# Performance work log

Hardware: AMD Instinct MI355X
Metric: run time of the kernel (lower is better)

Reference implementation:

```python
import jax, jax.numpy as jnp
import numpy as np

N = 100000   # nodes
E = 1600000  # edges
D = 128      # input_dim == hidden_dim
G = 64       # graphs in batch
EPS = 1e-5


def setup_inputs() -> dict:
    key = jax.random.key(0)
    ks = jax.random.split(key, 16)
    s = 1.0 / np.sqrt(D)
    inp = {
        "x": jax.random.normal(ks[0], (N, D), jnp.float32),
        "edge_index": jax.random.randint(ks[1], (2, E), 0, N, jnp.int64),
        "batch": jnp.sort(jax.random.randint(ks[2], (N,), 0, G, jnp.int64)),
        # 4 blocks x 2 SAGEConv layers = 8 convs, all DxD
        "Wl": jax.random.normal(ks[3], (8, D, D), jnp.float32) * s,
        "bl": jnp.zeros((8, D), jnp.float32),
        "Wr": jax.random.normal(ks[4], (8, D, D), jnp.float32) * s,
        "gamma": jnp.ones((4, D), jnp.float32),
        "beta": jnp.zeros((4, D), jnp.float32),
        # classifier: 2D -> D -> D//2 -> 1
        "W1": jax.random.normal(ks[5], (2 * D, D), jnp.float32) / np.sqrt(2 * D),
        "b1": jnp.zeros((D,), jnp.float32),
        "W2": jax.random.normal(ks[6], (D, D // 2), jnp.float32) * s,
        "b2": jnp.zeros((D // 2,), jnp.float32),
        "W3": jax.random.normal(ks[7], (D // 2, 1), jnp.float32) / np.sqrt(D // 2),
        "b3": jnp.zeros((1,), jnp.float32),
    }
    return inp


def _sage_conv(h, src, dst, inv_deg, W_l, b_l, W_r):
    # mean-aggregate neighbor features (messages flow src -> dst)
    agg = jax.ops.segment_sum(h[src], dst, num_segments=N) * inv_deg
    return agg @ W_l + b_l + h @ W_r


def _forward(x, edge_index, batch, Wl, bl, Wr, gamma, beta, W1, b1, W2, b2, W3, b3):
    src, dst = edge_index[0], edge_index[1]
    deg = jax.ops.segment_sum(jnp.ones((E,), x.dtype), dst, num_segments=N)
    inv_deg = (1.0 / jnp.maximum(deg, 1.0))[:, None]  # [N,1]

    h = x
    for blk in range(4):
        # GraphSAGE(in, hid, num_layers=2): conv -> relu -> conv
        h = _sage_conv(h, src, dst, inv_deg, Wl[2 * blk], bl[2 * blk], Wr[2 * blk])
        h = jax.nn.relu(h)
        h = _sage_conv(h, src, dst, inv_deg, Wl[2 * blk + 1], bl[2 * blk + 1], Wr[2 * blk + 1])
        # BatchNorm1d over nodes (training-mode batch statistics, biased var)
        mu = jnp.mean(h, axis=0)
        var = jnp.var(h, axis=0)
        h = (h - mu) * jax.lax.rsqrt(var + EPS) * gamma[blk] + beta[blk]
        h = jax.nn.relu(h)  # dropout is identity in eval mode

    # global mean / max pool over graph ids
    cnt = jax.ops.segment_sum(jnp.ones((N,), h.dtype), batch, num_segments=G)
    x_mean = jax.ops.segment_sum(h, batch, num_segments=G) / jnp.maximum(cnt, 1.0)[:, None]
    x_max = jax.ops.segment_max(h, batch, num_segments=G)
    g = jnp.concatenate([x_mean, x_max], axis=1)  # [G, 2D]

    g = jax.nn.relu(g @ W1 + b1)
    g = jax.nn.relu(g @ W2 + b2)
    return g @ W3 + b3  # [G, 1]


def reference(x, edge_index, batch, Wl, bl, Wr, gamma, beta, W1, b1, W2, b2, W3, b3):
    return _forward(x, edge_index, batch, Wl, bl, Wr, gamma, beta, W1, b1, W2, b2, W3, b3)
```

## Files before the change

kernel.cpp:

```cpp
#include <hip/hip_runtime.h>
#include <hip/hip_bf16.h>
#include <math.h>

#define NN 100000
#define NE 1600000
#define DIM 128
#define NG 64
#define EPSBN 1e-5f
#define NBLK 782
#define SORT_WIN 12500
#define NBINBLK 6250
#define DSL 64

typedef unsigned int u32;
typedef unsigned short u16;
typedef __attribute__((ext_vector_type(8))) short bf8_t;
typedef __attribute__((ext_vector_type(4))) float f4_t;
typedef __attribute__((ext_vector_type(4))) unsigned short u16x4;
#define MFMA(a, b, c) __builtin_amdgcn_mfma_f32_16x16x32_bf16((a), (b), (c), 0, 0, 0)

__device__ __forceinline__ u16 f2bf(float f) {
    u32 u = __float_as_uint(f);
    u32 r = u + 0x7FFFu + ((u >> 16) & 1u);
    return (u16)(r >> 16);
}
__device__ __forceinline__ float bf2f(u16 h) { return __uint_as_float(((u32)h) << 16); }

__global__ void k_bin_cnt(const int* __restrict__ ei, int* __restrict__ blkcnt) {
    __shared__ int c[8];
    int t = threadIdx.x;
    if (t < 8) c[t] = 0;
    __syncthreads();
    int e = blockIdx.x * 256 + t;
    int d = ei[NE + e];
    atomicAdd(&c[d / SORT_WIN], 1);
    __syncthreads();
    if (t < 8) blkcnt[blockIdx.x * 8 + t] = c[t];
}

__global__ void k_bin_scan(const int* __restrict__ blkcnt, int* __restrict__ blkoff,
                           int* __restrict__ wtotal) {
    __shared__ int ps[256];
    int w = blockIdx.x, t = threadIdx.x;
    const int PER = (NBINBLK + 255) / 256;
    int s = 0;
    for (int i = 0; i < PER; ++i) {
        int b = t * PER + i;
        if (b < NBINBLK) s += blkcnt[b * 8 + w];
    }
    ps[t] = s;
    for (int off = 1; off < 256; off <<= 1) {
        __syncthreads();
        int x = (t >= off) ? ps[t - off] : 0;
        __syncthreads();
        ps[t] += x;
    }
    __syncthreads();
    int run = (t ? ps[t - 1] : 0);
    for (int i = 0; i < PER; ++i) {
        int b = t * PER + i;
        if (b < NBINBLK) { blkoff[b * 8 + w] = run; run += blkcnt[b * 8 + w]; }
    }
    if (t == 255) wtotal[w] = ps[255];
}

__global__ void k_bin_start(const int* __restrict__ wtotal, int* __restrict__ binStart) {
    if (threadIdx.x == 0) {
        int a = 0;
        for (int w = 0; w < 8; ++w) { binStart[w] = a; a += wtotal[w]; }
        binStart[8] = a;
    }
}

__global__ void k_bin_place(const int* __restrict__ ei, const int* __restrict__ blkoff,
                            const int* __restrict__ binStart, int2* __restrict__ binned) {
    __shared__ int base[8];
    int t = threadIdx.x;
    if (t < 8) base[t] = binStart[t] + blkoff[blockIdx.x * 8 + t];
    __syncthreads();
    int e = blockIdx.x * 256 + t;
    int s = ei[e], d = ei[NE + e];
    int pos = atomicAdd(&base[d / SORT_WIN], 1);
    binned[pos] = make_int2(s, d);
}

__global__ void k_deg2(const int2* __restrict__ binned, const int* __restrict__ binStart,
                       int* __restrict__ deg) {
    int w = blockIdx.x & 7, sl = blockIdx.x >> 3;
    int b0 = binStart[w], b1 = binStart[w + 1];
    int chunk = (b1 - b0 + DSL - 1) / DSL;
    int r0 = b0 + sl * chunk, r1 = min(r0 + chunk, b1);
    for (int i = r0 + threadIdx.x; i < r1; i += 256)
        atomicAdd(&deg[binned[i].y], 1);
}

__global__ void k_scatter(const int2* __restrict__ binned, const int* __restrict__ binStart,
                          int* __restrict__ cursor, int* __restrict__ sorted_src) {
    int w = blockIdx.x & 7, sl = blockIdx.x >> 3;
    int b0 = binStart[w], b1 = binStart[w + 1];
    int chunk = (b1 - b0 + DSL - 1) / DSL;
    int r0 = b0 + sl * chunk, r1 = min(r0 + chunk, b1);
    for (int i = r0 + threadIdx.x; i < r1; i += 256) {
        int2 e = binned[i];
        int pos = atomicAdd(&cursor[e.y], 1);
        sorted_src[pos] = e.x;
    }
}

#define SCAN_B 256
__global__ void k_scan1(const int* __restrict__ deg, int* __restrict__ row_start,
                        int* __restrict__ bsum, float* __restrict__ inv_deg) {
    __shared__ int s[SCAN_B];
    int t = threadIdx.x;
    int i = blockIdx.x * SCAN_B + t;
    int v = (i < NN) ? deg[i] : 0;
    if (i < NN) inv_deg[i] = 1.0f / (float)(v > 1 ? v : 1);
    s[t] = v;
    for (int off = 1; off < SCAN_B; off <<= 1) {
        __syncthreads();
        int x = (t >= off) ? s[t - off] : 0;
        __syncthreads();
        s[t] += x;
    }
    if (i < NN) row_start[i + 1] = s[t];
    if (t == SCAN_B - 1) bsum[blockIdx.x] = s[t];
}

__global__ void k_scan2(int* __restrict__ bsum, int nb) {
    __shared__ int s[512];
    int t = threadIdx.x;
    int v = (t < nb) ? bsum[t] : 0;
    s[t] = v;
    for (int off = 1; off < 512; off <<= 1) {
        __syncthreads();
        int x = (t >= off) ? s[t - off] : 0;
        __syncthreads();
        s[t] += x;
    }
    if (t < nb) bsum[t] = s[t] - v;
}

__global__ void k_scan3(int* __restrict__ row_start, const int* __restrict__ bsum,
                        int* __restrict__ cursor) {
    int i = blockIdx.x * blockDim.x + threadIdx.x;
    if (i < NN) {
        int v = row_start[i + 1] + bsum[i / SCAN_B];
        row_start[i + 1] = v;
        if (i + 1 < NN) cursor[i + 1] = v;
    }
    if (i == 0) { row_start[0] = 0; cursor[0] = 0; }
}

__global__ void k_bounds(const int* __restrict__ batch, int* __restrict__ gs) {
    int g = threadIdx.x;
    if (g > NG) return;
    int lo = 0, hi = NN;
    while (lo < hi) {
        int mid = (lo + hi) >> 1;
        if (batch[mid] < g) lo = mid + 1; else hi = mid;
    }
    gs[g] = lo;
}

__global__ void k_split_x(const float* __restrict__ x, u16* __restrict__ Xh,
                          u16* __restrict__ Xl) {
    int idx = blockIdx.x * 256 + threadIdx.x;
    int base = idx * 4;
    float4 v = *reinterpret_cast<const float4*>(&x[base]);
    u16x4 hi, lo;
    float vv[4] = {v.x, v.y, v.z, v.w};
#pragma unroll
    for (int j = 0; j < 4; j++) {
        u16 h = f2bf(vv[j]);
        hi[j] = h;
        lo[j] = f2bf(vv[j] - bf2f(h));
    }
    *reinterpret_cast<u16x4*>(&Xh[base]) = hi;
    *reinterpret_cast<u16x4*>(&Xl[base]) = lo;
}

__global__ void k_prep_w(const float* __restrict__ Wl, const float* __restrict__ Wr,
                         u16* __restrict__ Wth, u16* __restrict__ Wtl) {
    int idx = blockIdx.x * 256 + threadIdx.x;
    int k = idx & 255;
    int col = (idx >> 8) & 127;
    int c = idx >> 15;
    float v = (k < 128) ? Wl[(c * 128 + k) * 128 + col] : Wr[(c * 128 + (k - 128)) * 128 + col];
    u16 h = f2bf(v);
    Wth[idx] = h;
    Wtl[idx] = f2bf(v - bf2f(h));
}

template <int AFF>
__global__ void k_aggregate(const u16* __restrict__ Hh,
                            const int* __restrict__ row_start, const int* __restrict__ ssrc,
                            const float* __restrict__ inv_deg, const float* __restrict__ ss,
                            u16* __restrict__ Ah, u16* __restrict__ Al) {
    int wid = blockIdx.x * 4 + (threadIdx.x >> 6);
    int lane = threadIdx.x & 63;
    int half = lane >> 5;
    int cl = lane & 31;
    if (wid >= NN) return;
    float sc0 = 0.f, sc1 = 0.f, sc2 = 0.f, sc3 = 0.f;
    float sh0 = 0.f, sh1 = 0.f, sh2 = 0.f, sh3 = 0.f;
    if (AFF) {
        float4 s4 = *reinterpret_cast<const float4*>(ss + cl * 4);
        float4 h4 = *reinterpret_cast<const float4*>(ss + 128 + cl * 4);
        sc0 = s4.x; sc1 = s4.y; sc2 = s4.z; sc3 = s4.w;
        sh0 = h4.x; sh1 = h4.y; sh2 = h4.z; sh3 = h4.w;
    }
    int beg = row_start[wid], end = row_start[wid + 1];
    int n = end - beg;
    float a0 = 0.f, a1 = 0.f, a2 = 0.f, a3 = 0.f;
#define ACCUM(vv)                                                                   \
    {                                                                               \
        float t0 = __uint_as_float((vv).x << 16);                                   \
        float t1 = __uint_as_float((vv).x & 0xFFFF0000u);                           \
        float t2 = __uint_as_float((vv).y << 16);                                   \
        float t3 = __uint_as_float((vv).y & 0xFFFF0000u);                           \
        if (AFF) {                                                                  \
            t0 = fmaxf(t0 * sc0 + sh0, 0.f); t1 = fmaxf(t1 * sc1 + sh1, 0.f);       \
            t2 = fmaxf(t2 * sc2 + sh2, 0.f); t3 = fmaxf(t3 * sc3 + sh3, 0.f);       \
        }                                                                           \
        a0 += t0; a1 += t1; a2 += t2; a3 += t3;                                     \
    }
    for (int base = 0; base < n; base += 64) {
        int rem = n - base;
        int idx = beg + base + (lane < rem ? lane : 0);
        int sv = ssrc[idx];
        int m = rem < 64 ? rem : 64;
        int j = 0;
        for (; j + 4 <= m; j += 4) {
            int sA = __shfl(sv, j + half);
            int sB = __shfl(sv, j + 2 + half);
            uint2 vA = *reinterpret_cast<const uint2*>(
                reinterpret_cast<const u32*>(Hh + (size_t)sA * DIM) + cl * 2);
            uint2 vB = *reinterpret_cast<const uint2*>(
                reinterpret_cast<const u32*>(Hh + (size_t)sB * DIM) + cl * 2);
            ACCUM(vA); ACCUM(vB);
        }
        for (; j < m; j += 2) {
            if (j + half < m) {
                int s0 = __shfl(sv, j + half);
                uint2 v = *reinterpret_cast<const uint2*>(
                    reinterpret_cast<const u32*>(Hh + (size_t)s0 * DIM) + cl * 2);
                ACCUM(v);
            }
        }
    }
#undef ACCUM
    a0 += __shfl_down(a0, 32);
    a1 += __shfl_down(a1, 32);
    a2 += __shfl_down(a2, 32);
    a3 += __shfl_down(a3, 32);
    if (half == 0) {
        float sc = inv_deg[wid];
        a0 *= sc; a1 *= sc; a2 *= sc; a3 *= sc;
        u16 h0 = f2bf(a0), h1 = f2bf(a1), h2 = f2bf(a2), h3 = f2bf(a3);
        u16 l0 = f2bf(a0 - bf2f(h0)), l1 = f2bf(a1 - bf2f(h1));
        u16 l2 = f2bf(a2 - bf2f(h2)), l3 = f2bf(a3 - bf2f(h3));
        uint2 hv = make_uint2((u32)h0 | ((u32)h1 << 16), (u32)h2 | ((u32)h3 << 16));
        uint2 lv = make_uint2((u32)l0 | ((u32)l1 << 16), (u32)l2 | ((u32)l3 << 16));
        *reinterpret_cast<uint2*>(Ah + (size_t)wid * DIM + cl * 4) = hv;
        *reinterpret_cast<uint2*>(Al + (size_t)wid * DIM + cl * 4) = lv;
    }
}

__device__ __forceinline__ void affine_split(bf8_t& h, bf8_t& l,
                                             const float* __restrict__ ss, int k0) {
#pragma unroll
    for (int j = 0; j < 8; ++j) {
        float v = bf2f((u16)h[j]) + bf2f((u16)l[j]);
        v = fmaxf(v * ss[k0 + j] + ss[128 + k0 + j], 0.f);
        u16 hh = f2bf(v);
        h[j] = (short)hh;
        l[j] = (short)f2bf(v - bf2f(hh));
    }
}

template <bool RELU, bool STATS, bool AFF2>
__global__ __launch_bounds__(256) void k_gemm(
    const u16* __restrict__ A1h, const u16* __restrict__ A1l,
    const u16* __restrict__ A2h, const u16* __restrict__ A2l,
    const u16* __restrict__ Wth, const u16* __restrict__ Wtl,
    const float* __restrict__ bias, const float* __restrict__ ss,
    u16* __restrict__ Oh, u16* __restrict__ Ol,
    float* __restrict__ partials) {
    __shared__ float cs[128], cq[128];
    int t = threadIdx.x;
    if (STATS) {
        if (t < 128) { cs[t] = 0.f; cq[t] = 0.f; }
        __syncthreads();
    }
    int w = t >> 6, l = t & 63;
    int rl = l & 15, kg = l >> 4;
    int rbase = blockIdx.x * 128 + w * 32;
    int row0 = rbase + rl, row1 = rbase + 16 + rl;
    int row0c = min(row0, NN - 1), row1c = min(row1, NN - 1);

    f4_t acc[2][8];
#pragma unroll
    for (int i = 0; i < 2; i++)
#pragma unroll
        for (int j = 0; j < 8; j++) acc[i][j] = (f4_t){0.f, 0.f, 0.f, 0.f};

#pragma unroll
    for (int ks = 0; ks < 4; ++ks) {
        int k0 = ks * 32 + kg * 8;
        bf8_t a0h = *reinterpret_cast<const bf8_t*>(A1h + row0c * DIM + k0);
        bf8_t a0l = *reinterpret_cast<const bf8_t*>(A1l + row0c * DIM + k0);
        bf8_t a1h = *reinterpret_cast<const bf8_t*>(A1h + row1c * DIM + k0);
        bf8_t a1l = *reinterpret_cast<const bf8_t*>(A1l + row1c * DIM + k0);
#pragma unroll
        for (int cf = 0; cf < 8; ++cf) {
            int wo = (cf * 16 + rl) * 256 + k0;
            bf8_t bh = *reinterpret_cast<const bf8_t*>(Wth + wo);
            bf8_t bl_ = *reinterpret_cast<const bf8_t*>(Wtl + wo);
            acc[0][cf] = MFMA(a0h, bh, acc[0][cf]);
            acc[0][cf] = MFMA(a0h, bl_, acc[0][cf]);
            acc[0][cf] = MFMA(a0l, bh, acc[0][cf]);
            acc[1][cf] = MFMA(a1h, bh, acc[1][cf]);
            acc[1][cf] = MFMA(a1h, bl_, acc[1][cf]);
            acc[1][cf] = MFMA(a1l, bh, acc[1][cf]);
        }
    }
#pragma unroll
    for (int ks = 0; ks < 4; ++ks) {
        int k0 = ks * 32 + kg * 8;
        bf8_t a0h = *reinterpret_cast<const bf8_t*>(A2h + row0c * DIM + k0);
        bf8_t a0l = *reinterpret_cast<const bf8_t*>(A2l + row0c * DIM + k0);
        bf8_t a1h = *reinterpret_cast<const bf8_t*>(A2h + row1c * DIM + k0);
        bf8_t a1l = *reinterpret_cast<const bf8_t*>(A2l + row1c * DIM + k0);
        if (AFF2) {
            affine_split(a0h, a0l, ss, k0);
            affine_split(a1h, a1l, ss, k0);
        }
#pragma unroll
        for (int cf = 0; cf < 8; ++cf) {
            int wo = (cf * 16 + rl) * 256 + 128 + k0;
            bf8_t bh = *reinterpret_cast<const bf8_t*>(Wth + wo);
            bf8_t bl_ = *reinterpret_cast<const bf8_t*>(Wtl + wo);
            acc[0][cf] = MFMA(a0h, bh, acc[0][cf]);
            acc[0][cf] = MFMA(a0h, bl_, acc[0][cf]);
            acc[0][cf] = MFMA(a0l, bh, acc[0][cf]);
            acc[1][cf] = MFMA(a1h, bh, acc[1][cf]);
            acc[1][cf] = MFMA(a1h, bl_, acc[1][cf]);
            acc[1][cf] = MFMA(a1l, bh, acc[1][cf]);
        }
    }

#pragma unroll
    for (int rf = 0; rf < 2; ++rf) {
        int rb = rbase + rf * 16 + kg * 4;
#pragma unroll
        for (int cf = 0; cf < 8; ++cf) {
            int col = cf * 16 + rl;
            float bv = bias[col];
            float s = 0.f, q = 0.f;
#pragma unroll
            for (int i = 0; i < 4; ++i) {
                int row = rb + i;
                float v = acc[rf][cf][i] + bv;
                if (RELU) v = fmaxf(v, 0.f);
                if (row < NN) {
                    u16 hi = f2bf(v);
                    Oh[row * DIM + col] = hi;
                    Ol[row * DIM + col] = f2bf(v - bf2f(hi));
                    if (STATS) { s += v; q += v * v; }
                }
            }
            if (STATS) {
                s += __shfl_xor(s, 16); s += __shfl_xor(s, 32);
                q += __shfl_xor(q, 16); q += __shfl_xor(q, 32);
                if (l < 16) {
                    atomicAdd(&cs[col], s);
                    atomicAdd(&cq[col], q);
                }
            }
        }
    }
    if (STATS) {
        __syncthreads();
        partials[blockIdx.x * 256 + t] = (t < 128) ? cs[t] : cq[t - 128];
    }
}

__global__ void k_bn_r1(const float* __restrict__ partials, float* __restrict__ colpart) {
    int t = threadIdx.x;
    int b = blockIdx.x;
    int b0 = b * 25, b1 = min(b0 + 25, NBLK);
    float s = 0.f;
    for (int i = b0; i < b1; ++i) s += partials[i * 256 + t];
    colpart[b * 256 + t] = s;
}

__global__ void k_bn_r2(const float* __restrict__ colpart, const float* __restrict__ gamma,
                        const float* __restrict__ beta, float* __restrict__ scaleshift) {
    __shared__ float sm[256];
    int t = threadIdx.x;
    float s = 0.f;
#pragma unroll
    for (int b = 0; b < 32; ++b) s += colpart[b * 256 + t];
    sm[t] = s;
    __syncthreads();
    if (t < 128) {
        float mu = sm[t] * (1.0f / NN);
        float var = sm[t + 128] * (1.0f / NN) - mu * mu;
        float sc = rsqrtf(var + EPSBN) * gamma[t];
        scaleshift[t] = sc;
        scaleshift[t + 128] = beta[t] - mu * sc;
    }
}

__global__ void k_pool(const u16* __restrict__ Hh, const int* __restrict__ gs,
                       const float* __restrict__ ss,
                       float* __restrict__ pSum, float* __restrict__ pMax) {
    int g = blockIdx.x >> 3, slice = blockIdx.x & 7;
    int s0 = gs[g], s1 = gs[g + 1];
    int len = s1 - s0;
    int chunk = (len + 7) >> 3;
    int r0 = s0 + slice * chunk;
    int r1 = min(r0 + chunk, s1);
    int t = threadIdx.x;
    int c2 = (t & 63) * 2, half = t >> 6;
    float sc0 = ss[c2], sc1 = ss[c2 + 1];
    float sh0 = ss[128 + c2], sh1 = ss[128 + c2 + 1];
    float sa = 0.f, sb = 0.f, ma = 0.f, mb = 0.f;
    for (int r = r0 + half; r < r1; r += 4) {
        u32 h2 = *reinterpret_cast<const u32*>(Hh + r * DIM + c2);
        float v0 = fmaxf(__uint_as_float(h2 << 16) * sc0 + sh0, 0.f);
        float v1 = fmaxf(__uint_as_float(h2 & 0xFFFF0000u) * sc1 + sh1, 0.f);
        sa += v0; sb += v1;
        ma = fmaxf(ma, v0); mb = fmaxf(mb, v1);
    }
    __shared__ float ls[4][128], lm[4][128];
    ls[half][c2] = sa; ls[half][c2 + 1] = sb;
    lm[half][c2] = ma; lm[half][c2 + 1] = mb;
    __syncthreads();
    if (t < 128) {
        float s = ls[0][t] + ls[1][t] + ls[2][t] + ls[3][t];
        float m = fmaxf(fmaxf(lm[0][t], lm[1][t]), fmaxf(lm[2][t], lm[3][t]));
        atomicAdd(&pSum[g * DIM + t], s);
        atomicMax((int*)&pMax[g * DIM + t], __float_as_int(m));
    }
}

__global__ void k_mlp(const float* __restrict__ pSum, const float* __restrict__ pMax,
                      const int* __restrict__ gs,
                      const float* __restrict__ W1, const float* __restrict__ b1,
                      const float* __restrict__ W2, const float* __restrict__ b2,
                      const float* __restrict__ W3, const float* __restrict__ b3,
                      float* __restrict__ out) {
    __shared__ float g[256], y1[128], y2[64];
    int gi = blockIdx.x;
    int t = threadIdx.x;
    int cnt = gs[gi + 1] - gs[gi];
    float inv = 1.0f / fmaxf((float)cnt, 1.0f);
    g[t] = pSum[gi * DIM + t] * inv;
    g[128 + t] = pMax[gi * DIM + t];
    __syncthreads();
    float a = b1[t];
    for (int k = 0; k < 256; k++) a += g[k] * W1[k * 128 + t];
    y1[t] = fmaxf(a, 0.f);
    __syncthreads();
    if (t < 64) {
        float a2 = b2[t];
        for (int k = 0; k < 128; k++) a2 += y1[k] * W2[k * 64 + t];
        y2[t] = fmaxf(a2, 0.f);
    }
    __syncthreads();
    if (t < 64) {
        float p = y2[t] * W3[t];
#pragma unroll
        for (int off = 32; off; off >>= 1) p += __shfl_down(p, off);
        if (t == 0) out[gi] = p + b3[0];
    }
}

extern "C" void kernel_launch(void* const* d_in, const int* in_sizes, int n_in,
                              void* d_out, int out_size, void* d_ws, size_t ws_size,
                              hipStream_t stream) {
    const float* x     = (const float*)d_in[0];
    const int*   ei    = (const int*)d_in[1];
    const int*   batch = (const int*)d_in[2];
    const float* Wl    = (const float*)d_in[3];
    const float* bl    = (const float*)d_in[4];
    const float* Wr    = (const float*)d_in[5];
    const float* gamma = (const float*)d_in[6];
    const float* beta  = (const float*)d_in[7];
    const float* W1    = (const float*)d_in[8];
    const float* b1    = (const float*)d_in[9];
    const float* W2    = (const float*)d_in[10];
    const float* b2    = (const float*)d_in[11];
    const float* W3    = (const float*)d_in[12];
    const float* b3    = (const float*)d_in[13];
    float* out = (float*)d_out;

    char* p = (char*)d_ws;
    size_t off = 0;
    auto alloc = [&](size_t bytes) -> void* {
        void* r = p + off;
        off += (bytes + 255) & ~(size_t)255;
        return r;
    };
    const size_t HB = (size_t)NN * DIM * 2;
    u16* Xh   = (u16*)alloc(HB);
    u16* Xl   = (u16*)alloc(HB);
    u16* hAh  = (u16*)alloc(HB);
    u16* hAl  = (u16*)alloc(HB);
    u16* aggh = (u16*)alloc(HB);
    u16* aggl = (u16*)alloc(HB);
    int*   ssrc      = (int*)alloc((size_t)NE * 4);
    u16*   Wth       = (u16*)alloc((size_t)8 * 128 * 256 * 2);
    u16*   Wtl       = (u16*)alloc((size_t)8 * 128 * 256 * 2);
    float* partials  = (float*)alloc((size_t)NBLK * 256 * 4);
    float* colpart   = (float*)alloc(32 * 256 * 4);
    int*   deg       = (int*)alloc(NN * 4);
    float* inv_deg   = (float*)alloc(NN * 4);
    int*   row_start = (int*)alloc((NN + 1) * 4);
    int*   cursor    = (int*)alloc(NN * 4);
    int*   bsum      = (int*)alloc(512 * 4);
    int*   gs        = (int*)alloc((NG + 1) * 4);
    int*   blkcnt    = (int*)alloc((size_t)NBINBLK * 8 * 4);
    int*   blkoff    = (int*)alloc((size_t)NBINBLK * 8 * 4);
    int*   wtotal    = (int*)alloc(8 * 4);
    int*   binStart  = (int*)alloc(9 * 4);
    float* ssb       = (float*)alloc(4 * 256 * 4);
    float* pSum      = (float*)alloc(NG * DIM * 4);
    float* pMax      = (float*)alloc(NG * DIM * 4);
    int2*  binned    = (int2*)aggh;

    const int nbN = (NN + 255) / 256;
    const int nbQ = NN * DIM / 4 / 256;
    const int aggGrid = (NN + 3) / 4;

    hipMemsetAsync(deg, 0, NN * 4, stream);
    k_bin_cnt<<<NBINBLK, 256, 0, stream>>>(ei, blkcnt);
    k_bin_scan<<<8, 256, 0, stream>>>(blkcnt, blkoff, wtotal);
    k_bin_start<<<1, 64, 0, stream>>>(wtotal, binStart);
    k_bin_place<<<NBINBLK, 256, 0, stream>>>(ei, blkoff, binStart, binned);
    k_deg2<<<8 * DSL, 256, 0, stream>>>(binned, binStart, deg);
    k_scan1<<<nbN, 256, 0, stream>>>(deg, row_start, bsum, inv_deg);
    k_scan2<<<1, 512, 0, stream>>>(bsum, nbN);
    k_scan3<<<nbN, 256, 0, stream>>>(row_start, bsum, cursor);
    k_scatter<<<8 * DSL, 256, 0, stream>>>(binned, binStart, cursor, ssrc);
    k_bounds<<<1, 128, 0, stream>>>(batch, gs);

    k_split_x<<<nbQ, 256, 0, stream>>>(x, Xh, Xl);
    k_prep_w<<<8 * 128 * 256 / 256, 256, 0, stream>>>(Wl, Wr, Wth, Wtl);

    for (int b = 0; b < 4; b++) {
        int c0 = 2 * b, c1 = 2 * b + 1;
        const u16* W0h = Wth + (size_t)c0 * 128 * 256;
        const u16* W0l = Wtl + (size_t)c0 * 128 * 256;
        const u16* W1h = Wth + (size_t)c1 * 128 * 256;
        const u16* W1l = Wtl + (size_t)c1 * 128 * 256;
        const float* ssPrev = ssb + (size_t)(b > 0 ? b - 1 : 0) * 256;
        if (b == 0) {
            k_aggregate<0><<<aggGrid, 256, 0, stream>>>(Xh, row_start, ssrc, inv_deg,
                                                        ssPrev, aggh, aggl);
            k_gemm<true, false, false><<<NBLK, 256, 0, stream>>>(
                aggh, aggl, Xh, Xl, W0h, W0l, bl + c0 * DIM, ssPrev, hAh, hAl, partials);
        } else {
            k_aggregate<1><<<aggGrid, 256, 0, stream>>>(Xh, row_start, ssrc, inv_deg,
                                                        ssPrev, aggh, aggl);
            k_gemm<true, false, true><<<NBLK, 256, 0, stream>>>(
                aggh, aggl, Xh, Xl, W0h, W0l, bl + c0 * DIM, ssPrev, hAh, hAl, partials);
        }
        k_aggregate<0><<<aggGrid, 256, 0, stream>>>(hAh, row_start, ssrc, inv_deg,
                                                    ssPrev, aggh, aggl);
        k_gemm<false, true, false><<<NBLK, 256, 0, stream>>>(
            aggh, aggl, hAh, hAl, W1h, W1l, bl + c1 * DIM, ssPrev, Xh, Xl, partials);
        k_bn_r1<<<32, 256, 0, stream>>>(partials, colpart);
        k_bn_r2<<<1, 256, 0, stream>>>(colpart, gamma + b * DIM, beta + b * DIM,
                                       ssb + (size_t)b * 256);
    }

    hipMemsetAsync(pSum, 0, NG * DIM * 4, stream);
    hipMemsetAsync(pMax, 0, NG * DIM * 4, stream);
    k_pool<<<NG * 8, 256, 0, stream>>>(Xh, gs, ssb + 3 * 256, pSum, pMax);
    k_mlp<<<NG, 128, 0, stream>>>(pSum, pMax, gs, W1, b1, W2, b2, W3, b3, out);
}
```

Baseline: 1.662 ms.

## Restructure GEMM tiling: per-wave column slices with register-resident weights and double-buffered A loads

The GEMM kernel now gives each block 64 rows, and each of its four waves a 32-column slice, instead of each wave owning 32 rows and all 128 columns. Each wave keeps its weight slice (hi/lo bf16, full K=256) in registers, and the A-operand loads are double-buffered across K chunks so loads overlap with MFMA work. The grid doubles to 1563 blocks with a 2-blocks-per-CU launch bound, and the BN partial reduction is resized to match. This trades repeated weight reloads for higher register pressure and reading each A row from four waves.

```diff
diff --git a/kernel.cpp b/kernel.cpp
--- a/kernel.cpp
+++ b/kernel.cpp
@@ -7,7 +7,7 @@
 #define DIM 128
 #define NG 64
 #define EPSBN 1e-5f
-#define NBLK 782
+#define NGB 1563
 #define SORT_WIN 12500
 #define NBINBLK 6250
 #define DSL 64
@@ -279,7 +279,7 @@
 }
 
 template <bool RELU, bool STATS, bool AFF2>
-__global__ __launch_bounds__(256) void k_gemm(
+__global__ __launch_bounds__(256, 2) void k_gemm(
     const u16* __restrict__ A1h, const u16* __restrict__ A1l,
     const u16* __restrict__ A2h, const u16* __restrict__ A2l,
     const u16* __restrict__ Wth, const u16* __restrict__ Wtl,
@@ -288,107 +288,124 @@
     float* __restrict__ partials) {
     __shared__ float cs[128], cq[128];
     int t = threadIdx.x;
-    if (STATS) {
-        if (t < 128) { cs[t] = 0.f; cq[t] = 0.f; }
-        __syncthreads();
-    }
     int w = t >> 6, l = t & 63;
     int rl = l & 15, kg = l >> 4;
-    int rbase = blockIdx.x * 128 + w * 32;
-    int row0 = rbase + rl, row1 = rbase + 16 + rl;
-    int row0c = min(row0, NN - 1), row1c = min(row1, NN - 1);
-
-    f4_t acc[2][8];
-#pragma unroll
-    for (int i = 0; i < 2; i++)
-#pragma unroll
-        for (int j = 0; j < 8; j++) acc[i][j] = (f4_t){0.f, 0.f, 0.f, 0.f};
-
-#pragma unroll
-    for (int ks = 0; ks < 4; ++ks) {
-        int k0 = ks * 32 + kg * 8;
-        bf8_t a0h = *reinterpret_cast<const bf8_t*>(A1h + row0c * DIM + k0);
-        bf8_t a0l = *reinterpret_cast<const bf8_t*>(A1l + row0c * DIM + k0);
-        bf8_t a1h = *reinterpret_cast<const bf8_t*>(A1h + row1c * DIM + k0);
-        bf8_t a1l = *reinterpret_cast<const bf8_t*>(A1l + row1c * DIM + k0);
-#pragma unroll
-        for (int cf = 0; cf < 8; ++cf) {
-            int wo = (cf * 16 + rl) * 256 + k0;
-            bf8_t bh = *reinterpret_cast<const bf8_t*>(Wth + wo);
-            bf8_t bl_ = *reinterpret_cast<const bf8_t*>(Wtl + wo);
-            acc[0][cf] = MFMA(a0h, bh, acc[0][cf]);
-            acc[0][cf] = MFMA(a0h, bl_, acc[0][cf]);
-            acc[0][cf] = MFMA(a0l, bh, acc[0][cf]);
-            acc[1][cf] = MFMA(a1h, bh, acc[1][cf]);
-            acc[1][cf] = MFMA(a1h, bl_, acc[1][cf]);
-            acc[1][cf] = MFMA(a1l, bh, acc[1][cf]);
+    int col0 = w * 32;
+    int rbase = blockIdx.x * 64;
+    int rc0 = min(rbase + rl, NN - 1);
+    int rc1 = min(rbase + 16 + rl, NN - 1);
+    int rc2 = min(rbase + 32 + rl, NN - 1);
+    int rc3 = min(rbase + 48 + rl, NN - 1);
+
+    bf8_t wh[2][8], wlo[2][8];
+#pragma unroll
+    for (int cf = 0; cf < 2; ++cf) {
+        const u16* pw = Wth + (size_t)(col0 + cf * 16 + rl) * 256 + kg * 8;
+        const u16* pl = Wtl + (size_t)(col0 + cf * 16 + rl) * 256 + kg * 8;
+#pragma unroll
+        for (int kc = 0; kc < 8; ++kc) {
+            wh[cf][kc] = *reinterpret_cast<const bf8_t*>(pw + kc * 32);
+            wlo[cf][kc] = *reinterpret_cast<const bf8_t*>(pl + kc * 32);
         }
     }
-#pragma unroll
-    for (int ks = 0; ks < 4; ++ks) {
-        int k0 = ks * 32 + kg * 8;
-        bf8_t a0h = *reinterpret_cast<const bf8_t*>(A2h + row0c * DIM + k0);
-        bf8_t a0l = *reinterpret_cast<const bf8_t*>(A2l + row0c * DIM + k0);
-        bf8_t a1h = *reinterpret_cast<const bf8_t*>(A2h + row1c * DIM + k0);
-        bf8_t a1l = *reinterpret_cast<const bf8_t*>(A2l + row1c * DIM + k0);
-        if (AFF2) {
-            affine_split(a0h, a0l, ss, k0);
-            affine_split(a1h, a1l, ss, k0);
-        }
-#pragma unroll
-        for (int cf = 0; cf < 8; ++cf) {
-            int wo = (cf * 16 + rl) * 256 + 128 + k0;
-            bf8_t bh = *reinterpret_cast<const bf8_t*>(Wth + wo);
-            bf8_t bl_ = *reinterpret_cast<const bf8_t*>(Wtl + wo);
-            acc[0][cf] = MFMA(a0h, bh, acc[0][cf]);
-            acc[0][cf] = MFMA(a0h, bl_, acc[0][cf]);
-            acc[0][cf] = MFMA(a0l, bh, acc[0][cf]);
-            acc[1][cf] = MFMA(a1h, bh, acc[1][cf]);
-            acc[1][cf] = MFMA(a1h, bl_, acc[1][cf]);
-            acc[1][cf] = MFMA(a1l, bh, acc[1][cf]);
-        }
-    }
-
-#pragma unroll
-    for (int rf = 0; rf < 2; ++rf) {
-        int rb = rbase + rf * 16 + kg * 4;
-#pragma unroll
-        for (int cf = 0; cf < 8; ++cf) {
-            int col = cf * 16 + rl;
-            float bv = bias[col];
-            float s = 0.f, q = 0.f;
-#pragma unroll
-            for (int i = 0; i < 4; ++i) {
-                int row = rb + i;
-                float v = acc[rf][cf][i] + bv;
+
+    f4_t acc[4][2];
+#pragma unroll
+    for (int i = 0; i < 4; ++i)
+#pragma unroll
+        for (int j = 0; j < 2; ++j) acc[i][j] = (f4_t){0.f, 0.f, 0.f, 0.f};
+
+    bf8_t aH[4], aL[4], bH[4], bL[4];
+
+#define LOADK(kc, H, L)                                                          \
+    {                                                                            \
+        const u16* _bh = ((kc) < 4) ? A1h : A2h;                                 \
+        const u16* _bl = ((kc) < 4) ? A1l : A2l;                                 \
+        int _ko = ((kc) & 3) * 32 + kg * 8;                                      \
+        H[0] = *reinterpret_cast<const bf8_t*>(_bh + (size_t)rc0 * DIM + _ko);   \
+        L[0] = *reinterpret_cast<const bf8_t*>(_bl + (size_t)rc0 * DIM + _ko);   \
+        H[1] = *reinterpret_cast<const bf8_t*>(_bh + (size_t)rc1 * DIM + _ko);   \
+        L[1] = *reinterpret_cast<const bf8_t*>(_bl + (size_t)rc1 * DIM + _ko);   \
+        H[2] = *reinterpret_cast<const bf8_t*>(_bh + (size_t)rc2 * DIM + _ko);   \
+        L[2] = *reinterpret_cast<const bf8_t*>(_bl + (size_t)rc2 * DIM + _ko);   \
+        H[3] = *reinterpret_cast<const bf8_t*>(_bh + (size_t)rc3 * DIM + _ko);   \
+        L[3] = *reinterpret_cast<const bf8_t*>(_bl + (size_t)rc3 * DIM + _ko);   \
+    }
+
+#define COMPK(kc, H, L)                                                          \
+    {                                                                            \
+        if (AFF2 && (kc) >= 4) {                                                 \
+            int _k0 = ((kc) - 4) * 32 + kg * 8;                                  \
+            affine_split(H[0], L[0], ss, _k0);                                   \
+            affine_split(H[1], L[1], ss, _k0);                                   \
+            affine_split(H[2], L[2], ss, _k0);                                   \
+            affine_split(H[3], L[3], ss, _k0);                                   \
+        }                                                                        \
+        _Pragma("unroll")                                                        \
+        for (int _rf = 0; _rf < 4; ++_rf) {                                      \
+            _Pragma("unroll")                                                    \
+            for (int _cf = 0; _cf < 2; ++_cf) {                                  \
+                acc[_rf][_cf] = MFMA(H[_rf], wh[_cf][(kc)], acc[_rf][_cf]);      \
+                acc[_rf][_cf] = MFMA(H[_rf], wlo[_cf][(kc)], acc[_rf][_cf]);     \
+                acc[_rf][_cf] = MFMA(L[_rf], wh[_cf][(kc)], acc[_rf][_cf]);      \
+            }                                                                    \
+        }                                                                        \
+    }
+
+    LOADK(0, aH, aL)
+    LOADK(1, bH, bL) COMPK(0, aH, aL)
+    LOADK(2, aH, aL) COMPK(1, bH, bL)
+    LOADK(3, bH, bL) COMPK(2, aH, aL)
+    LOADK(4, aH, aL) COMPK(3, bH, bL)
+    LOADK(5, bH, bL) COMPK(4, aH, aL)
+    LOADK(6, aH, aL) COMPK(5, bH, bL)
+    LOADK(7, bH, bL) COMPK(6, aH, aL)
+    COMPK(7, bH, bL)
+#undef LOADK
+#undef COMPK
+
+    float bv0 = bias[col0 + rl];
+    float bv1 = bias[col0 + 16 + rl];
+    float s0 = 0.f, q0 = 0.f, s1 = 0.f, q1 = 0.f;
+#pragma unroll
+    for (int rf = 0; rf < 4; ++rf) {
+#pragma unroll
+        for (int i = 0; i < 4; ++i) {
+            int row = rbase + rf * 16 + kg * 4 + i;
+            if (row < NN) {
+                float v = acc[rf][0][i] + bv0;
                 if (RELU) v = fmaxf(v, 0.f);
-                if (row < NN) {
-                    u16 hi = f2bf(v);
-                    Oh[row * DIM + col] = hi;
-                    Ol[row * DIM + col] = f2bf(v - bf2f(hi));
-                    if (STATS) { s += v; q += v * v; }
-                }
-            }
-            if (STATS) {
-                s += __shfl_xor(s, 16); s += __shfl_xor(s, 32);
-                q += __shfl_xor(q, 16); q += __shfl_xor(q, 32);
-                if (l < 16) {
-                    atomicAdd(&cs[col], s);
-                    atomicAdd(&cq[col], q);
-                }
+                u16 hi = f2bf(v);
+                Oh[(size_t)row * DIM + col0 + rl] = hi;
+                Ol[(size_t)row * DIM + col0 + rl] = f2bf(v - bf2f(hi));
+                if (STATS) { s0 += v; q0 += v * v; }
+                float v1 = acc[rf][1][i] + bv1;
+                if (RELU) v1 = fmaxf(v1, 0.f);
+                u16 hi1 = f2bf(v1);
+                Oh[(size_t)row * DIM + col0 + 16 + rl] = hi1;
+                Ol[(size_t)row * DIM + col0 + 16 + rl] = f2bf(v1 - bf2f(hi1));
+                if (STATS) { s1 += v1; q1 += v1 * v1; }
             }
         }
     }
     if (STATS) {
+        s0 += __shfl_xor(s0, 16); s0 += __shfl_xor(s0, 32);
+        q0 += __shfl_xor(q0, 16); q0 += __shfl_xor(q0, 32);
+        s1 += __shfl_xor(s1, 16); s1 += __shfl_xor(s1, 32);
+        q1 += __shfl_xor(q1, 16); q1 += __shfl_xor(q1, 32);
+        if (l < 16) {
+            cs[col0 + rl] = s0; cq[col0 + rl] = q0;
+            cs[col0 + 16 + rl] = s1; cq[col0 + 16 + rl] = q1;
+        }
         __syncthreads();
-        partials[blockIdx.x * 256 + t] = (t < 128) ? cs[t] : cq[t - 128];
+        partials[(size_t)blockIdx.x * 256 + t] = (t < 128) ? cs[t] : cq[t - 128];
     }
 }
 
 __global__ void k_bn_r1(const float* __restrict__ partials, float* __restrict__ colpart) {
     int t = threadIdx.x;
     int b = blockIdx.x;
-    int b0 = b * 25, b1 = min(b0 + 25, NBLK);
+    int b0 = b * 49, b1 = min(b0 + 49, NGB);
     float s = 0.f;
     for (int i = b0; i < b1; ++i) s += partials[i * 256 + t];
     colpart[b * 256 + t] = s;
@@ -513,7 +530,7 @@
     int*   ssrc      = (int*)alloc((size_t)NE * 4);
     u16*   Wth       = (u16*)alloc((size_t)8 * 128 * 256 * 2);
     u16*   Wtl       = (u16*)alloc((size_t)8 * 128 * 256 * 2);
-    float* partials  = (float*)alloc((size_t)NBLK * 256 * 4);
+    float* partials  = (float*)alloc((size_t)NGB * 256 * 4);
     float* colpart   = (float*)alloc(32 * 256 * 4);
     int*   deg       = (int*)alloc(NN * 4);
     float* inv_deg   = (float*)alloc(NN * 4);
@@ -559,17 +576,17 @@
         if (b == 0) {
             k_aggregate<0><<<aggGrid, 256, 0, stream>>>(Xh, row_start, ssrc, inv_deg,
                                                         ssPrev, aggh, aggl);
-            k_gemm<true, false, false><<<NBLK, 256, 0, stream>>>(
+            k_gemm<true, false, false><<<NGB, 256, 0, stream>>>(
                 aggh, aggl, Xh, Xl, W0h, W0l, bl + c0 * DIM, ssPrev, hAh, hAl, partials);
         } else {
             k_aggregate<1><<<aggGrid, 256, 0, stream>>>(Xh, row_start, ssrc, inv_deg,
                                                         ssPrev, aggh, aggl);
-            k_gemm<true, false, true><<<NBLK, 256, 0, stream>>>(
+            k_gemm<true, false, true><<<NGB, 256, 0, stream>>>(
                 aggh, aggl, Xh, Xl, W0h, W0l, bl + c0 * DIM, ssPrev, hAh, hAl, partials);
         }
         k_aggregate<0><<<aggGrid, 256, 0, stream>>>(hAh, row_start, ssrc, inv_deg,
                                                     ssPrev, aggh, aggl);
-        k_gemm<false, true, false><<<NBLK, 256, 0, stream>>>(
+        k_gemm<false, true, false><<<NGB, 256, 0, stream>>>(
             aggh, aggl, hAh, hAl, W1h, W1l, bl + c1 * DIM, ssPrev, Xh, Xl, partials);
         k_bn_r1<<<32, 256, 0, stream>>>(partials, colpart);
         k_bn_r2<<<1, 256, 0, stream>>>(colpart, gamma + b * DIM, beta + b * DIM,
```

After: 1.646 ms. No clear change (-1.0%).
